# Performance work log

Hardware: AMD Instinct MI355X
Metric: run time of the kernel (lower is better)

Reference implementation:

```python
import jax, jax.numpy as jnp
import numpy as np

N_NODES, N_EDGES, N_GRAPHS = 65536, 131072, 2048
F_NODE, F_EDGE, DIM, DIM1, DIM2 = 78, 10, 256, 512, 256
FP_DIM, FP2, FP3, NCB = 1489, 128, 256, 2

PNAMES = []
for _l in (1, 2, 3):
    PNAMES += [f"e{_l}w", f"e{_l}b", f"n{_l}w1", f"n{_l}b1", f"n{_l}w2", f"n{_l}b2",
               f"bn{_l}g", f"bn{_l}b", f"bn{_l}m", f"bn{_l}v"]
PNAMES += ["fcg_w", "fcg_b", "fp1_w", "fp1_b", "fp2_w", "fp2_b",
           "fb1_w", "fb1_b", "fb2_w", "fb2_b", "fb3_w", "fb3_b", "fb4_w", "fb4_b"]


def _params(key):
    ks = iter(jax.random.split(key, 64))
    def rn(*s):
        return jax.random.normal(next(ks), s, dtype=jnp.float32) * 0.05
    def ru(*s):
        return jax.random.uniform(next(ks), s, dtype=jnp.float32)
    p = {}
    for l, ci in zip((1, 2, 3), (F_NODE, DIM1, DIM1)):
        h = DIM if l == 1 else DIM1
        p[f"e{l}w"] = rn(ci, F_EDGE); p[f"e{l}b"] = rn(ci)          # GINEConv edge lin: 10 -> in_channels
        p[f"n{l}w1"] = rn(h, ci);     p[f"n{l}b1"] = rn(h)
        p[f"n{l}w2"] = rn(DIM1, h);   p[f"n{l}b2"] = rn(DIM1)
        p[f"bn{l}g"] = ru(DIM1) + 0.5; p[f"bn{l}b"] = rn(DIM1)
        p[f"bn{l}m"] = rn(DIM1);       p[f"bn{l}v"] = ru(DIM1) + 0.5
    p["fcg_w"] = rn(DIM2, DIM1);  p["fcg_b"] = rn(DIM2)
    p["fp1_w"] = rn(FP2, FP_DIM); p["fp1_b"] = rn(FP2)
    p["fp2_w"] = rn(FP3, FP2);    p["fp2_b"] = rn(FP3)
    for i, (o, ci) in enumerate([(256, 512), (128, 256), (64, 128), (NCB, 64)], 1):
        p[f"fb{i}_w"] = rn(o, ci); p[f"fb{i}_b"] = rn(o)
    return p


def setup_inputs() -> dict:
    key = jax.random.key(0)
    k = jax.random.split(key, 6)
    inp = {
        "x": jax.random.normal(k[0], (N_NODES, F_NODE), dtype=jnp.float32),
        "finger": jax.random.uniform(k[1], (N_GRAPHS, FP_DIM), dtype=jnp.float32),
        "edge_attr": jax.random.normal(k[2], (N_EDGES, F_EDGE), dtype=jnp.float32),
        "edge_index": jax.random.randint(k[3], (2, N_EDGES), 0, N_NODES),
        "batch": jnp.sort(jax.random.randint(k[4], (N_NODES,), 0, N_GRAPHS)),
    }
    inp.update(_params(k[5]))
    return inp


def _lin(x, w, b):
    return x @ w.T + b


def _bn(x, g, b, m, v):
    # eval-mode BatchNorm1d with running stats
    return (x - m) * jax.lax.rsqrt(v + 1e-5) * g + b


def _forward(x, finger, edge_attr, edge_index, batch, p):
    src, dst = edge_index[0], edge_index[1]
    h = x
    for l in (1, 2, 3):
        # GINEConv (eps=0): out = nn(x + sum_j relu(x_j + lin(edge_attr)))
        e = _lin(edge_attr, p[f"e{l}w"], p[f"e{l}b"])               # [E, Cin]
        m = jax.nn.relu(h[src] + e)                                   # gather + edge add
        agg = jax.ops.segment_sum(m, dst, num_segments=N_NODES)      # scatter-add
        t = h + agg
        t = _lin(jax.nn.relu(_lin(t, p[f"n{l}w1"], p[f"n{l}b1"])), p[f"n{l}w2"], p[f"n{l}b2"])
        h = _bn(jax.nn.relu(t), p[f"bn{l}g"], p[f"bn{l}b"], p[f"bn{l}m"], p[f"bn{l}v"])
    g = jax.ops.segment_sum(h, batch, num_segments=N_GRAPHS)         # global_add_pool
    g = jax.nn.relu(_lin(g, p["fcg_w"], p["fcg_b"]))                 # fc_1 (dropout is eval no-op)
    fp = jax.nn.relu(_lin(finger, p["fp1_w"], p["fp1_b"]))
    fp = jax.nn.relu(_lin(fp, p["fp2_w"], p["fp2_b"]))
    y = jnp.concatenate([g, fp], axis=1)                              # [B, 512]
    for i in (1, 2, 3):
        y = jax.nn.relu(_lin(y, p[f"fb{i}_w"], p[f"fb{i}_b"]))
    y = _lin(y, p["fb4_w"], p["fb4_b"])
    return jax.nn.sigmoid(y)


def reference(x, finger, edge_attr, edge_index, batch,
              e1w, e1b, n1w1, n1b1, n1w2, n1b2, bn1g, bn1b, bn1m, bn1v,
              e2w, e2b, n2w1, n2b1, n2w2, n2b2, bn2g, bn2b, bn2m, bn2v,
              e3w, e3b, n3w1, n3b1, n3w2, n3b2, bn3g, bn3b, bn3m, bn3v,
              fcg_w, fcg_b, fp1_w, fp1_b, fp2_w, fp2_b,
              fb1_w, fb1_b, fb2_w, fb2_b, fb3_w, fb3_b, fb4_w, fb4_b):
    args = dict(locals())
    p = {k: args[k] for k in PNAMES}
    return _forward(x, finger, edge_attr, edge_index, batch, p)
```

## Files before the change

kernel.cpp:

```cpp
#include <hip/hip_runtime.h>
#include <stdint.h>

typedef unsigned short u16;
typedef unsigned int u32;
typedef __bf16 bf16x8 __attribute__((ext_vector_type(8)));
typedef float f32x4 __attribute__((ext_vector_type(4)));
typedef _Float16 h2 __attribute__((ext_vector_type(2)));

#define N_NODES 65536
#define N_EDGES 131072
#define N_GRAPHS 2048

static __device__ __forceinline__ float bf2f(u16 u) {
  union { u32 u; float f; } v; v.u = ((u32)u) << 16; return v.f;
}
static __device__ __forceinline__ u16 f2bf(float f) {
  union { float f; u32 u; } v; v.f = f;
  u32 r = v.u + 0x7fffu + ((v.u >> 16) & 1u);
  return (u16)(r >> 16);
}
static __device__ __forceinline__ void gl16(const void* g, void* l) {
  __builtin_amdgcn_global_load_lds(
      (__attribute__((address_space(1))) void*)(g),
      (__attribute__((address_space(3))) void*)(l), 16, 0, 0);
}
static __device__ __forceinline__ h2 b2h2(u32 u) {
  union { u32 u; h2 h; } v; v.u = u; return v.h;
}
static __device__ __forceinline__ u32 pk2h(float a, float b) {
  union { _Float16 h[2]; u32 u; } v;
  v.h[0] = (_Float16)a; v.h[1] = (_Float16)b; return v.u;
}
#if __has_builtin(__builtin_amdgcn_fdot2)
#define FDOT2(a, b, c) __builtin_amdgcn_fdot2((a), (b), (c), false)
#else
#define FDOT2(a, b, c) \
  ((c) + (float)(a)[0] * (float)(b)[0] + (float)(a)[1] * (float)(b)[1])
#endif

template <int EPI>
__global__ __launch_bounds__(256) void gemm_bt128(
    const u16* __restrict__ A, const u16* __restrict__ W,
    const float* __restrict__ bias, const float* __restrict__ scale,
    const float* __restrict__ shift, u16* __restrict__ Cp,
    int K, int ldc) {
  __shared__ u16 As[128 * 128];
  __shared__ u16 Bs[128 * 128];
  const u32 gx = gridDim.x;
  const u32 nwg = gx * gridDim.y;
  u32 lid = blockIdx.y * gx + blockIdx.x;
  if ((nwg & 7u) == 0u) {
    const u32 cpx = nwg >> 3;
    lid = (lid & 7u) * cpx + (lid >> 3);
  }
  const int bm = (int)(lid / gx) * 128;
  const int bn = (int)(lid % gx) * 128;
  const int tid = threadIdx.x;
  const int lane = tid & 63;
  const int wid = tid >> 6;
  const int wr = wid >> 1, wc = wid & 1;
  const int lg = lane >> 4, lr = lane & 15;

  f32x4 acc[4][4];
#pragma unroll
  for (int i = 0; i < 4; ++i)
#pragma unroll
    for (int j = 0; j < 4; ++j) acc[i][j] = (f32x4){0.f, 0.f, 0.f, 0.f};

  const int srow16 = tid >> 4;
  const int gslot = ((tid & 15) ^ srow16) * 8;
  const u16* Ag[8];
  const u16* Wg[8];
#pragma unroll
  for (int p = 0; p < 8; ++p) {
    Ag[p] = A + (size_t)(bm + p * 16 + srow16) * K + gslot;
    Wg[p] = W + (size_t)(bn + p * 16 + srow16) * K + gslot;
  }
  u16* dA = &As[tid * 8];
  u16* dB = &Bs[tid * 8];

  for (int k0 = 0; k0 < K; k0 += 128) {
#pragma unroll
    for (int p = 0; p < 8; ++p) {
      gl16(Ag[p] + k0, dA + p * 2048);
      gl16(Wg[p] + k0, dB + p * 2048);
    }
    __syncthreads();
#pragma unroll
    for (int kk = 0; kk < 4; ++kk) {
      const int slot = ((kk * 4 + lg) ^ lr) * 8;
      bf16x8 af[4], bfv[4];
#pragma unroll
      for (int i = 0; i < 4; ++i)
        af[i] = *(const bf16x8*)&As[(wr * 64 + i * 16 + lr) * 128 + slot];
#pragma unroll
      for (int j = 0; j < 4; ++j)
        bfv[j] = *(const bf16x8*)&Bs[(wc * 64 + j * 16 + lr) * 128 + slot];
#pragma unroll
      for (int i = 0; i < 4; ++i)
#pragma unroll
        for (int j = 0; j < 4; ++j)
          acc[i][j] = __builtin_amdgcn_mfma_f32_16x16x32_bf16(
              af[i], bfv[j], acc[i][j], 0, 0, 0);
    }
    __syncthreads();
  }

#pragma unroll
  for (int i = 0; i < 4; ++i) {
#pragma unroll
    for (int j = 0; j < 4; ++j) {
#pragma unroll
      for (int r = 0; r < 4; ++r) {
        const int grow = bm + wr * 64 + i * 16 + lg * 4 + r;
        const int gcol = bn + wc * 64 + j * 16 + lr;
        float v = acc[i][j][r] + bias[gcol];
        v = fmaxf(v, 0.f);
        if (EPI == 1) v = v * scale[gcol] + shift[gcol];
        Cp[(size_t)grow * ldc + gcol] = f2bf(v);
      }
    }
  }
}

template <int EPI>
__global__ __launch_bounds__(256) void gemm_bt(
    const u16* __restrict__ A, const u16* __restrict__ W,
    const float* __restrict__ bias, const float* __restrict__ scale,
    const float* __restrict__ shift, u16* __restrict__ Cp,
    int K, int ldc, int coff) {
  __shared__ u16 As[128 * 32];
  __shared__ u16 Bs[128 * 32];
  const u32 gx = gridDim.x;
  const u32 nwg = gx * gridDim.y;
  u32 lid = blockIdx.y * gx + blockIdx.x;
  if ((nwg & 7u) == 0u) {
    const u32 cpx = nwg >> 3;
    lid = (lid & 7u) * cpx + (lid >> 3);
  }
  const int bm = (int)(lid / gx) * 128;
  const int bn = (int)(lid % gx) * 128;
  const int tid = threadIdx.x;
  const int lane = tid & 63;
  const int wid = tid >> 6;
  const int wr = wid >> 1, wc = wid & 1;
  const int lg = lane >> 4, lr = lane & 15;

  f32x4 acc[4][4];
#pragma unroll
  for (int i = 0; i < 4; ++i)
#pragma unroll
    for (int j = 0; j < 4; ++j) acc[i][j] = (f32x4){0.f, 0.f, 0.f, 0.f};

  const int srow = tid >> 2;
  const int c8 = (tid & 3) * 8;
  const u16* Ag0 = A + (size_t)(bm + srow) * K + c8;
  const u16* Ag1 = A + (size_t)(bm + 64 + srow) * K + c8;
  const u16* Wg0 = W + (size_t)(bn + srow) * K + c8;
  const u16* Wg1 = W + (size_t)(bn + 64 + srow) * K + c8;
  u16* lA0 = &As[tid * 8];
  u16* lA1 = &As[2048 + tid * 8];
  u16* lB0 = &Bs[tid * 8];
  u16* lB1 = &Bs[2048 + tid * 8];

  for (int k0 = 0; k0 < K; k0 += 32) {
    gl16(Ag0 + k0, lA0);
    gl16(Ag1 + k0, lA1);
    gl16(Wg0 + k0, lB0);
    gl16(Wg1 + k0, lB1);
    __syncthreads();
    bf16x8 af[4], bfv[4];
#pragma unroll
    for (int i = 0; i < 4; ++i)
      af[i] = *(const bf16x8*)&As[(wr * 64 + i * 16 + lr) * 32 + lg * 8];
#pragma unroll
    for (int j = 0; j < 4; ++j)
      bfv[j] = *(const bf16x8*)&Bs[(wc * 64 + j * 16 + lr) * 32 + lg * 8];
#pragma unroll
    for (int i = 0; i < 4; ++i)
#pragma unroll
      for (int j = 0; j < 4; ++j)
        acc[i][j] = __builtin_amdgcn_mfma_f32_16x16x32_bf16(af[i], bfv[j],
                                                            acc[i][j], 0, 0, 0);
    __syncthreads();
  }

#pragma unroll
  for (int i = 0; i < 4; ++i) {
#pragma unroll
    for (int j = 0; j < 4; ++j) {
#pragma unroll
      for (int r = 0; r < 4; ++r) {
        const int grow = bm + wr * 64 + i * 16 + lg * 4 + r;
        const int gcol = bn + wc * 64 + j * 16 + lr;
        float v = acc[i][j][r] + bias[gcol];
        v = fmaxf(v, 0.f);
        if (EPI == 1) v = v * scale[gcol] + shift[gcol];
        Cp[(size_t)grow * ldc + coff + gcol] = f2bf(v);
      }
    }
  }
}

__global__ void hist_deg(const int* __restrict__ dst, int* __restrict__ deg) {
  int e = blockIdx.x * blockDim.x + threadIdx.x;
  if (e < N_EDGES) atomicAdd(&deg[dst[e]], 1);
}

__global__ __launch_bounds__(1024) void scan_rowptr(const int* __restrict__ deg,
                                                    int* __restrict__ rowptr) {
  __shared__ int lds[1024];
  const int t = threadIdx.x;
  const int base = t * 64;
  int s = 0;
  for (int i = 0; i < 64; ++i) s += deg[base + i];
  lds[t] = s;
  __syncthreads();
  for (int ofs = 1; ofs < 1024; ofs <<= 1) {
    int v = (t >= ofs) ? lds[t - ofs] : 0;
    __syncthreads();
    lds[t] += v;
    __syncthreads();
  }
  int run = (t == 0) ? 0 : lds[t - 1];
  for (int i = 0; i < 64; ++i) {
    rowptr[base + i] = run;
    run += deg[base + i];
  }
  if (t == 1023) rowptr[65536] = run;
}

__global__ void scatter_csr(const int* __restrict__ dst,
                            const int* __restrict__ rowptr,
                            int* __restrict__ deg, int* __restrict__ csr) {
  int e = blockIdx.x * blockDim.x + threadIdx.x;
  if (e >= N_EDGES) return;
  int d = dst[e];
  int pos = atomicSub(&deg[d], 1) - 1;
  csr[rowptr[d] + pos] = e;
}

__global__ void prep_edges(const int* __restrict__ csr,
                           const int* __restrict__ esrc,
                           const float* __restrict__ ea,
                           int* __restrict__ src_s, u32* __restrict__ ea16) {
  int i = blockIdx.x * blockDim.x + threadIdx.x;
  if (i >= N_EDGES) return;
  const int eid = csr[i];
  src_s[i] = esrc[eid];
  const float* er = ea + (size_t)eid * 10;
  u32* o = ea16 + (size_t)i * 5;
  o[0] = pk2h(er[0], er[1]);
  o[1] = pk2h(er[2], er[3]);
  o[2] = pk2h(er[4], er[5]);
  o[3] = pk2h(er[6], er[7]);
  o[4] = pk2h(er[8], er[9]);
}

__global__ void ew_h16(const float* __restrict__ ew1, const float* __restrict__ ew2,
                       const float* __restrict__ ew3, u32* __restrict__ o1,
                       u32* __restrict__ o2, u32* __restrict__ o3) {
  int i = blockIdx.x * blockDim.x + threadIdx.x;
  const float* src;
  u32* dst;
  if (i < 512) { src = ew2 + (size_t)i * 10; dst = o2 + i * 5; }
  else if (i < 1024) { src = ew3 + (size_t)(i - 512) * 10; dst = o3 + (i - 512) * 5; }
  else if (i < 1102) { src = ew1 + (size_t)(i - 1024) * 10; dst = o1 + (i - 1024) * 5; }
  else return;
#pragma unroll
  for (int k = 0; k < 5; ++k) dst[k] = pk2h(src[2 * k], src[2 * k + 1]);
}

__global__ __launch_bounds__(128) void gather512d(
    const int* __restrict__ rowptr, const int* __restrict__ src_s,
    const u32* __restrict__ ea16, const u32* __restrict__ ew16,
    const float* __restrict__ eb, const u16* __restrict__ H,
    u16* __restrict__ T) {
  const int t = threadIdx.x;
  const int c4 = t * 4;
  h2 w[4][5];
#pragma unroll
  for (int j = 0; j < 4; ++j)
#pragma unroll
    for (int k = 0; k < 5; ++k) w[j][k] = b2h2(ew16[(c4 + j) * 5 + k]);
  float eb4[4];
#pragma unroll
  for (int j = 0; j < 4; ++j) eb4[j] = eb[c4 + j];

  const int dend = blockIdx.x * 8 + 8;
  for (int d = blockIdx.x * 8; d < dend; ++d) {
    uint2 hv = *(const uint2*)&H[(size_t)d * 512 + c4];
    float a0 = bf2f((u16)(hv.x & 0xffffu)), a1 = bf2f((u16)(hv.x >> 16));
    float a2 = bf2f((u16)(hv.y & 0xffffu)), a3 = bf2f((u16)(hv.y >> 16));
    const int i1 = rowptr[d + 1];
#pragma unroll 2
    for (int i = rowptr[d]; i < i1; ++i) {
      const int s = src_s[i];
      const u32* ep = ea16 + (size_t)i * 5;
      const h2 e0 = b2h2(ep[0]), e1 = b2h2(ep[1]), e2 = b2h2(ep[2]),
               e3 = b2h2(ep[3]), e4 = b2h2(ep[4]);
      uint2 hs = *(const uint2*)&H[(size_t)s * 512 + c4];
      float h0 = bf2f((u16)(hs.x & 0xffffu)), h1 = bf2f((u16)(hs.x >> 16));
      float h2v = bf2f((u16)(hs.y & 0xffffu)), h3 = bf2f((u16)(hs.y >> 16));
      float l0 = eb4[0], l1 = eb4[1], l2 = eb4[2], l3 = eb4[3];
      l0 = FDOT2(e0, w[0][0], l0); l0 = FDOT2(e1, w[0][1], l0);
      l0 = FDOT2(e2, w[0][2], l0); l0 = FDOT2(e3, w[0][3], l0);
      l0 = FDOT2(e4, w[0][4], l0);
      l1 = FDOT2(e0, w[1][0], l1); l1 = FDOT2(e1, w[1][1], l1);
      l1 = FDOT2(e2, w[1][2], l1); l1 = FDOT2(e3, w[1][3], l1);
      l1 = FDOT2(e4, w[1][4], l1);
      l2 = FDOT2(e0, w[2][0], l2); l2 = FDOT2(e1, w[2][1], l2);
      l2 = FDOT2(e2, w[2][2], l2); l2 = FDOT2(e3, w[2][3], l2);
      l2 = FDOT2(e4, w[2][4], l2);
      l3 = FDOT2(e0, w[3][0], l3); l3 = FDOT2(e1, w[3][1], l3);
      l3 = FDOT2(e2, w[3][2], l3); l3 = FDOT2(e3, w[3][3], l3);
      l3 = FDOT2(e4, w[3][4], l3);
      a0 += fmaxf(h0 + l0, 0.f);
      a1 += fmaxf(h1 + l1, 0.f);
      a2 += fmaxf(h2v + l2, 0.f);
      a3 += fmaxf(h3 + l3, 0.f);
    }
    uint2 r;
    r.x = (u32)f2bf(a0) | ((u32)f2bf(a1) << 16);
    r.y = (u32)f2bf(a2) | ((u32)f2bf(a3) << 16);
    *(uint2*)&T[(size_t)d * 512 + c4] = r;
  }
}

__global__ __launch_bounds__(128) void gather78d(
    const int* __restrict__ rowptr, const int* __restrict__ src_s,
    const u32* __restrict__ ea16, const u32* __restrict__ ew16,
    const float* __restrict__ eb, const float* __restrict__ X,
    u16* __restrict__ T) {
  const int t = threadIdx.x;
  const bool act = t < 78;
  h2 w[5];
  float ebv = 0.f;
  if (act) {
#pragma unroll
    for (int k = 0; k < 5; ++k) w[k] = b2h2(ew16[t * 5 + k]);
    ebv = eb[t];
  }
  const int dend = blockIdx.x * 8 + 8;
  for (int d = blockIdx.x * 8; d < dend; ++d) {
    float acc = act ? X[(size_t)d * 78 + t] : 0.f;
    const int i1 = rowptr[d + 1];
    for (int i = rowptr[d]; i < i1; ++i) {
      const int s = src_s[i];
      const u32* ep = ea16 + (size_t)i * 5;
      const h2 e0 = b2h2(ep[0]), e1 = b2h2(ep[1]), e2 = b2h2(ep[2]),
               e3 = b2h2(ep[3]), e4 = b2h2(ep[4]);
      if (act) {
        float el = ebv;
        el = FDOT2(e0, w[0], el); el = FDOT2(e1, w[1], el);
        el = FDOT2(e2, w[2], el); el = FDOT2(e3, w[3], el);
        el = FDOT2(e4, w[4], el);
        acc += fmaxf(X[(size_t)s * 78 + t] + el, 0.f);
      }
    }
    if (t < 96) T[(size_t)d * 96 + t] = act ? f2bf(acc) : (u16)0;
  }
}

struct CvtJob { const float* in; u16* out; int cin; int cout; };
struct CvtJobs { CvtJob j[11]; int blk_ofs[12]; };

__global__ __launch_bounds__(256) void cvt_multi(CvtJobs jb, int njobs) {
  int b = blockIdx.x;
  int ji = 0;
  while (ji + 1 < njobs && b >= jb.blk_ofs[ji + 1]) ++ji;
  const CvtJob J = jb.j[ji];
  int idx = (b - jb.blk_ofs[ji]) * 256 + threadIdx.x;
  int r = idx / J.cout, c = idx - r * J.cout;
  int tot_blocks = jb.blk_ofs[ji + 1] - jb.blk_ofs[ji];
  if (idx >= tot_blocks * 256) return;
  if (idx >= ((tot_blocks * 256) / J.cout) * J.cout && c >= J.cout) return;
  J.out[idx] = (c < J.cin) ? f2bf(J.in[(size_t)r * J.cin + c]) : (u16)0;
}

struct BnJobs { const float* g[3]; const float* b[3]; const float* m[3];
                const float* v[3]; };
__global__ void bn_affine3(BnJobs p, float* __restrict__ bnS) {
  int i = blockIdx.x * blockDim.x + threadIdx.x;
  int l = i >> 9, c = i & 511;
  float s = p.g[l][c] * rsqrtf(p.v[l][c] + 1e-5f);
  bnS[l * 1024 + c] = s;
  bnS[l * 1024 + 512 + c] = p.b[l][c] - p.m[l][c] * s;
}

__global__ void seg_starts(const int* __restrict__ batch, int* __restrict__ start,
                           int n, int ngraphs) {
  int i = blockIdx.x * blockDim.x + threadIdx.x;
  if (i >= n) return;
  int b = batch[i];
  int prev = (i == 0) ? -1 : batch[i - 1];
  for (int g = prev + 1; g <= b; ++g) start[g] = i;
  if (i == n - 1)
    for (int g = b + 1; g <= ngraphs; ++g) start[g] = n;
}

__global__ void cvt_pad(const float* __restrict__ in, u16* __restrict__ out,
                        int rows, int cin, int cout) {
  int idx = blockIdx.x * blockDim.x + threadIdx.x;
  if (idx >= rows * cout) return;
  int rrow = idx / cout, j = idx - rrow * cout;
  out[idx] = (j < cin) ? f2bf(in[(size_t)rrow * cin + j]) : (u16)0;
}

__global__ void pool_sum(const u16* __restrict__ H, const int* __restrict__ start,
                         u16* __restrict__ g) {
  int gi = blockIdx.x, c = threadIdx.x;
  int s = start[gi], e = start[gi + 1];
  float acc = 0.f;
  for (int i = s; i < e; ++i) acc += bf2f(H[(size_t)i * 512 + c]);
  g[gi * 512 + c] = f2bf(acc);
}

__global__ void fb34(const u16* __restrict__ y2, const float* __restrict__ w3,
                     const float* __restrict__ b3, const float* __restrict__ w4,
                     const float* __restrict__ b4, float* __restrict__ out) {
  __shared__ float yr[128];
  __shared__ float h3[64];
  const int row = blockIdx.x, t = threadIdx.x;
  yr[t] = bf2f(y2[row * 128 + t]);
  yr[t + 64] = bf2f(y2[row * 128 + 64 + t]);
  __syncthreads();
  float s = b3[t];
  const float* w3r = &w3[t * 128];
#pragma unroll 8
  for (int k = 0; k < 128; ++k) s += yr[k] * w3r[k];
  h3[t] = fmaxf(s, 0.f);
  __syncthreads();
  if (t < 2) {
    float s4 = b4[t];
    const float* w4r = &w4[t * 64];
    for (int k = 0; k < 64; ++k) s4 += h3[k] * w4r[k];
    out[row * 2 + t] = 1.f / (1.f + expf(-s4));
  }
}

#define CDIV(a, b) (((a) + (b)-1) / (b))

extern "C" void kernel_launch(void* const* d_in, const int* in_sizes, int n_in,
                              void* d_out, int out_size, void* d_ws, size_t ws_size,
                              hipStream_t stream) {
  const float* x = (const float*)d_in[0];
  const float* finger = (const float*)d_in[1];
  const float* ea = (const float*)d_in[2];
  const int* eidx = (const int*)d_in[3];
  const int* batch = (const int*)d_in[4];
  const int* esrc = eidx;
  const int* edst = eidx + N_EDGES;

  const float* P[49];
  for (int i = 5; i < 49; ++i) P[i] = (const float*)d_in[i];
  const float* fcg_w = P[35]; const float* fcg_b = P[36];
  const float* fp1_w = P[37]; const float* fp1_b = P[38];
  const float* fp2_w = P[39]; const float* fp2_b = P[40];
  const float* fb1_w = P[41]; const float* fb1_b = P[42];
  const float* fb2_w = P[43]; const float* fb2_b = P[44];
  const float* fb3_w = P[45]; const float* fb3_b = P[46];
  const float* fb4_w = P[47]; const float* fb4_b = P[48];

  size_t off = 0;
  char* base = (char*)d_ws;
  auto alloc = [&](size_t bytes) -> void* {
    void* p = base + off;
    off = (off + bytes + 255) & ~(size_t)255;
    return p;
  };
  char* BA = (char*)alloc((size_t)N_NODES * 512 * 2);
  char* BB = (char*)alloc((size_t)N_NODES * 512 * 2);
  u16* w11 = (u16*)alloc(256 * 96 * 2);
  u16* w12 = (u16*)alloc(512 * 256 * 2);
  u16* w21 = (u16*)alloc(512 * 512 * 2);
  u16* w22 = (u16*)alloc(512 * 512 * 2);
  u16* w31 = (u16*)alloc(512 * 512 * 2);
  u16* w32 = (u16*)alloc(512 * 512 * 2);
  u16* wfcg = (u16*)alloc(256 * 512 * 2);
  u16* wfp1 = (u16*)alloc(128 * 1504 * 2);
  u16* wfp2 = (u16*)alloc(256 * 128 * 2);
  u16* wfb1 = (u16*)alloc(256 * 512 * 2);
  u16* wfb2 = (u16*)alloc(128 * 256 * 2);
  float* bnS = (float*)alloc(6 * 512 * 4);
  int* start = (int*)alloc(2049 * 4);
  int* deg = (int*)alloc(65536 * 4);
  int* rowptr = (int*)alloc(65537 * 4);
  int* csr = (int*)alloc(131072 * 4);
  int* src_s = (int*)alloc(131072 * 4);
  u32* ea16 = (u32*)alloc((size_t)131072 * 5 * 4);
  u32* ew16a = (u32*)alloc(512 * 5 * 4);
  u32* ew16b = (u32*)alloc(512 * 5 * 4);
  u32* ew16c = (u32*)alloc(128 * 5 * 4);
  if (off > ws_size) return;

  u16* fingb = (u16*)BA;
  u16* gbuf = (u16*)(BA + 6160384);
  u16* y0 = (u16*)(BA + 8257536);
  u16* fpa = (u16*)(BA + 10354688);
  u16* y1 = (u16*)(BA + 10878976);
  u16* y2 = (u16*)(BA + 11927552);

  {
    CvtJobs jb;
    const float* ins[11] = {P[5 + 2], P[5 + 4], P[15 + 2], P[15 + 4], P[25 + 2],
                            P[25 + 4], fcg_w, fp1_w, fp2_w, fb1_w, fb2_w};
    u16* outs[11] = {w11, w12, w21, w22, w31, w32, wfcg, wfp1, wfp2, wfb1, wfb2};
    int rows[11] = {256, 512, 512, 512, 512, 512, 256, 128, 256, 256, 128};
    int cins[11] = {78, 256, 512, 512, 512, 512, 512, 1489, 128, 512, 256};
    int couts[11] = {96, 256, 512, 512, 512, 512, 512, 1504, 128, 512, 256};
    int acc = 0;
    for (int i = 0; i < 11; ++i) {
      jb.j[i].in = ins[i]; jb.j[i].out = outs[i];
      jb.j[i].cin = cins[i]; jb.j[i].cout = couts[i];
      jb.blk_ofs[i] = acc;
      acc += CDIV(rows[i] * couts[i], 256);
    }
    jb.blk_ofs[11] = acc;
    cvt_multi<<<acc, 256, 0, stream>>>(jb, 11);
  }
  {
    BnJobs bj;
    for (int l = 0; l < 3; ++l) {
      int pb = 5 + 10 * l;
      bj.g[l] = P[pb + 6]; bj.b[l] = P[pb + 7];
      bj.m[l] = P[pb + 8]; bj.v[l] = P[pb + 9];
    }
    bn_affine3<<<6, 256, 0, stream>>>(bj, bnS);
  }
  seg_starts<<<CDIV(N_NODES, 256), 256, 0, stream>>>(batch, start, N_NODES, N_GRAPHS);
  ew_h16<<<5, 256, 0, stream>>>(P[5], P[15], P[25], ew16c, ew16a, ew16b);

  hipMemsetAsync(deg, 0, 65536 * 4, stream);
  hist_deg<<<CDIV(N_EDGES, 256), 256, 0, stream>>>(edst, deg);
  scan_rowptr<<<1, 1024, 0, stream>>>(deg, rowptr);
  scatter_csr<<<CDIV(N_EDGES, 256), 256, 0, stream>>>(edst, rowptr, deg, csr);
  prep_edges<<<CDIV(N_EDGES, 256), 256, 0, stream>>>(csr, esrc, ea, src_s, ea16);

  gather78d<<<N_NODES / 8, 128, 0, stream>>>(rowptr, src_s, ea16, ew16c, P[6], x,
                                             (u16*)BB);
  gemm_bt<0><<<dim3(2, 512), 256, 0, stream>>>((u16*)BB, w11, P[5 + 3], nullptr,
                                               nullptr, (u16*)BA, 96, 256, 0);
  gemm_bt128<1><<<dim3(4, 512), 256, 0, stream>>>((u16*)BA, w12, P[5 + 5], bnS,
                                                  bnS + 512, (u16*)BB, 256, 512);

  gather512d<<<N_NODES / 8, 128, 0, stream>>>(rowptr, src_s, ea16, ew16a, P[16],
                                              (const u16*)BB, (u16*)BA);
  gemm_bt128<0><<<dim3(4, 512), 256, 0, stream>>>((u16*)BA, w21, P[15 + 3], nullptr,
                                                  nullptr, (u16*)BB, 512, 512);
  gemm_bt128<1><<<dim3(4, 512), 256, 0, stream>>>((u16*)BB, w22, P[15 + 5],
                                                  bnS + 1024, bnS + 1024 + 512,
                                                  (u16*)BA, 512, 512);

  gather512d<<<N_NODES / 8, 128, 0, stream>>>(rowptr, src_s, ea16, ew16b, P[26],
                                              (const u16*)BA, (u16*)BB);
  gemm_bt128<0><<<dim3(4, 512), 256, 0, stream>>>((u16*)BB, w31, P[25 + 3], nullptr,
                                                  nullptr, (u16*)BA, 512, 512);
  gemm_bt128<1><<<dim3(4, 512), 256, 0, stream>>>((u16*)BA, w32, P[25 + 5],
                                                  bnS + 2048, bnS + 2048 + 512,
                                                  (u16*)BB, 512, 512);

  pool_sum<<<N_GRAPHS, 512, 0, stream>>>((const u16*)BB, start, gbuf);
  cvt_pad<<<CDIV(N_GRAPHS * 1504, 256), 256, 0, stream>>>(finger, fingb, N_GRAPHS,
                                                          1489, 1504);
  gemm_bt<0><<<dim3(2, 16), 256, 0, stream>>>(gbuf, wfcg, fcg_b, nullptr, nullptr,
                                              y0, 512, 512, 0);
  gemm_bt<0><<<dim3(1, 16), 256, 0, stream>>>(fingb, wfp1, fp1_b, nullptr, nullptr,
                                              fpa, 1504, 128, 0);
  gemm_bt<0><<<dim3(2, 16), 256, 0, stream>>>(fpa, wfp2, fp2_b, nullptr, nullptr,
                                              y0, 128, 512, 256);
  gemm_bt<0><<<dim3(2, 16), 256, 0, stream>>>(y0, wfb1, fb1_b, nullptr, nullptr,
                                              y1, 512, 256, 0);
  gemm_bt<0><<<dim3(1, 16), 256, 0, stream>>>(y1, wfb2, fb2_b, nullptr, nullptr,
                                              y2, 256, 128, 0);
  fb34<<<N_GRAPHS, 64, 0, stream>>>(y2, fb3_w, fb3_b, fb4_w, fb4_b, (float*)d_out);
}
```

Baseline: 536.5 us.

## Fuse graph-level MLP head into one kernel with LDS-resident intermediates

Replaces the six separate head launches (fc_g, two fingerprint linears, fb1, fb2, fb34) with a single kernel. Each 512-thread block handles 16 graphs and keeps intermediate activations in shared memory between MFMA stages. fb3 also moves to bf16 MFMA, which needs an extra weight conversion job. This removes launch overhead and global round-trips for the small head GEMMs. In exchange there are only 128 blocks, each re-reading weights directly from global memory, and fb3 runs at lower precision.

```diff
diff --git a/kernel.cpp b/kernel.cpp
--- a/kernel.cpp
+++ b/kernel.cpp
@@ -199,6 +199,132 @@
         Cp[(size_t)grow * ldc + coff + gcol] = f2bf(v);
       }
     }
+  }
+}
+
+static __device__ __forceinline__ void head_stage2(
+    const u16* Sa, u16* So, int kofs, const u16* __restrict__ W, int ldw,
+    const float* __restrict__ bias, int KT, int w, int l, int lr, int lg) {
+  f32x4 acc[2];
+  acc[0] = (f32x4){0.f, 0.f, 0.f, 0.f};
+  acc[1] = (f32x4){0.f, 0.f, 0.f, 0.f};
+  for (int t = 0; t < KT; ++t) {
+    bf16x8 a = *(const bf16x8*)&Sa[t * 512 + l * 8];
+#pragma unroll
+    for (int j = 0; j < 2; ++j) {
+      bf16x8 b = *(const bf16x8*)&W[(size_t)(w * 32 + j * 16 + lr) * ldw +
+                                    t * 32 + lg * 8];
+      acc[j] = __builtin_amdgcn_mfma_f32_16x16x32_bf16(b, a, acc[j], 0, 0, 0);
+    }
+  }
+#pragma unroll
+  for (int j = 0; j < 2; ++j) {
+    const int c0 = w * 32 + j * 16 + lg * 4;
+    const float4 bs = *(const float4*)&bias[c0];
+    const float v0 = fmaxf(acc[j][0] + bs.x, 0.f);
+    const float v1 = fmaxf(acc[j][1] + bs.y, 0.f);
+    const float v2 = fmaxf(acc[j][2] + bs.z, 0.f);
+    const float v3 = fmaxf(acc[j][3] + bs.w, 0.f);
+    uint2 r;
+    r.x = (u32)f2bf(v0) | ((u32)f2bf(v1) << 16);
+    r.y = (u32)f2bf(v2) | ((u32)f2bf(v3) << 16);
+    const int k0 = kofs + c0;
+    *(uint2*)&So[(k0 >> 5) * 512 + ((k0 & 31) >> 3) * 128 + lr * 8 + (k0 & 7)] = r;
+  }
+}
+
+static __device__ __forceinline__ void head_stage1(
+    const u16* Sa, u16* So, int kofs, const u16* __restrict__ W, int ldw,
+    const float* __restrict__ bias, int KT, int w, int l, int lr, int lg) {
+  f32x4 acc = (f32x4){0.f, 0.f, 0.f, 0.f};
+  for (int t = 0; t < KT; ++t) {
+    bf16x8 a = *(const bf16x8*)&Sa[t * 512 + l * 8];
+    bf16x8 b = *(const bf16x8*)&W[(size_t)(w * 16 + lr) * ldw + t * 32 + lg * 8];
+    acc = __builtin_amdgcn_mfma_f32_16x16x32_bf16(b, a, acc, 0, 0, 0);
+  }
+  const int c0 = w * 16 + lg * 4;
+  const float4 bs = *(const float4*)&bias[c0];
+  const float v0 = fmaxf(acc[0] + bs.x, 0.f);
+  const float v1 = fmaxf(acc[1] + bs.y, 0.f);
+  const float v2 = fmaxf(acc[2] + bs.z, 0.f);
+  const float v3 = fmaxf(acc[3] + bs.w, 0.f);
+  uint2 r;
+  r.x = (u32)f2bf(v0) | ((u32)f2bf(v1) << 16);
+  r.y = (u32)f2bf(v2) | ((u32)f2bf(v3) << 16);
+  const int k0 = kofs + c0;
+  *(uint2*)&So[(k0 >> 5) * 512 + ((k0 & 31) >> 3) * 128 + lr * 8 + (k0 & 7)] = r;
+}
+
+__global__ __launch_bounds__(512) void head_fused(
+    const u16* __restrict__ gbuf, const u16* __restrict__ fingb,
+    const u16* __restrict__ wfcg, const float* __restrict__ fcg_b,
+    const u16* __restrict__ wfp1, const float* __restrict__ fp1_b,
+    const u16* __restrict__ wfp2, const float* __restrict__ fp2_b,
+    const u16* __restrict__ wfb1, const float* __restrict__ fb1_b,
+    const u16* __restrict__ wfb2, const float* __restrict__ fb2_b,
+    const u16* __restrict__ wfb3, const float* __restrict__ fb3_b,
+    const float* __restrict__ fb4_w, const float* __restrict__ fb4_b,
+    float* __restrict__ out) {
+  __shared__ u16 S[26624];
+  const int g0 = blockIdx.x * 16;
+  const int tid = threadIdx.x;
+  const int w = tid >> 6, l = tid & 63;
+  const int lr = l & 15, lg = l >> 4;
+
+  for (int v = tid; v < 1024; v += 512) {
+    const int r = v >> 6, c0 = (v & 63) * 8;
+    uint4 d = *(const uint4*)&gbuf[(size_t)(g0 + r) * 512 + c0];
+    *(uint4*)&S[(c0 >> 5) * 512 + ((c0 & 31) >> 3) * 128 + r * 8] = d;
+  }
+  __syncthreads();
+  head_stage2(&S[0], &S[8192], 0, wfcg, 512, fcg_b, 16, w, l, lr, lg);
+  {
+    f32x4 acc = (f32x4){0.f, 0.f, 0.f, 0.f};
+    for (int t = 0; t < 47; ++t) {
+      bf16x8 a = *(const bf16x8*)&fingb[(size_t)(g0 + lr) * 1504 + t * 32 + lg * 8];
+      bf16x8 b = *(const bf16x8*)&wfp1[(size_t)(w * 16 + lr) * 1504 + t * 32 + lg * 8];
+      acc = __builtin_amdgcn_mfma_f32_16x16x32_bf16(b, a, acc, 0, 0, 0);
+    }
+    const int c0 = w * 16 + lg * 4;
+    const float4 bs = *(const float4*)&fp1_b[c0];
+    const float v0 = fmaxf(acc[0] + bs.x, 0.f);
+    const float v1 = fmaxf(acc[1] + bs.y, 0.f);
+    const float v2 = fmaxf(acc[2] + bs.z, 0.f);
+    const float v3 = fmaxf(acc[3] + bs.w, 0.f);
+    uint2 r;
+    r.x = (u32)f2bf(v0) | ((u32)f2bf(v1) << 16);
+    r.y = (u32)f2bf(v2) | ((u32)f2bf(v3) << 16);
+    *(uint2*)&S[16384 + (c0 >> 5) * 512 + ((c0 & 31) >> 3) * 128 + lr * 8 +
+                (c0 & 7)] = r;
+  }
+  __syncthreads();
+  head_stage2(&S[16384], &S[8192], 256, wfp2, 128, fp2_b, 4, w, l, lr, lg);
+  __syncthreads();
+  head_stage2(&S[8192], &S[18432], 0, wfb1, 512, fb1_b, 16, w, l, lr, lg);
+  __syncthreads();
+  head_stage1(&S[18432], &S[22528], 0, wfb2, 256, fb2_b, 8, w, l, lr, lg);
+  __syncthreads();
+  if (w < 4) {
+    f32x4 acc = (f32x4){0.f, 0.f, 0.f, 0.f};
+    for (int t = 0; t < 4; ++t) {
+      bf16x8 a = *(const bf16x8*)&S[22528 + t * 512 + l * 8];
+      bf16x8 b = *(const bf16x8*)&wfb3[(size_t)(w * 16 + lr) * 128 + t * 32 + lg * 8];
+      acc = __builtin_amdgcn_mfma_f32_16x16x32_bf16(b, a, acc, 0, 0, 0);
+    }
+    const int c0 = w * 16 + lg * 4;
+    float* H3 = (float*)&S[24576];
+#pragma unroll
+    for (int r = 0; r < 4; ++r)
+      H3[lr * 64 + c0 + r] = fmaxf(acc[r] + fb3_b[c0 + r], 0.f);
+  }
+  __syncthreads();
+  if (tid < 32) {
+    const int r = tid >> 1, o = tid & 1;
+    const float* H3 = (const float*)&S[24576];
+    float s = fb4_b[o];
+#pragma unroll 8
+    for (int k = 0; k < 64; ++k) s += H3[r * 64 + k] * fb4_w[o * 64 + k];
+    out[(size_t)(g0 + r) * 2 + o] = 1.f / (1.f + expf(-s));
   }
 }
 
@@ -363,7 +489,7 @@
 }
 
 struct CvtJob { const float* in; u16* out; int cin; int cout; };
-struct CvtJobs { CvtJob j[11]; int blk_ofs[12]; };
+struct CvtJobs { CvtJob j[12]; int blk_ofs[13]; };
 
 __global__ __launch_bounds__(256) void cvt_multi(CvtJobs jb, int njobs) {
   int b = blockIdx.x;
@@ -414,29 +540,6 @@
   float acc = 0.f;
   for (int i = s; i < e; ++i) acc += bf2f(H[(size_t)i * 512 + c]);
   g[gi * 512 + c] = f2bf(acc);
-}
-
-__global__ void fb34(const u16* __restrict__ y2, const float* __restrict__ w3,
-                     const float* __restrict__ b3, const float* __restrict__ w4,
-                     const float* __restrict__ b4, float* __restrict__ out) {
-  __shared__ float yr[128];
-  __shared__ float h3[64];
-  const int row = blockIdx.x, t = threadIdx.x;
-  yr[t] = bf2f(y2[row * 128 + t]);
-  yr[t + 64] = bf2f(y2[row * 128 + 64 + t]);
-  __syncthreads();
-  float s = b3[t];
-  const float* w3r = &w3[t * 128];
-#pragma unroll 8
-  for (int k = 0; k < 128; ++k) s += yr[k] * w3r[k];
-  h3[t] = fmaxf(s, 0.f);
-  __syncthreads();
-  if (t < 2) {
-    float s4 = b4[t];
-    const float* w4r = &w4[t * 64];
-    for (int k = 0; k < 64; ++k) s4 += h3[k] * w4r[k];
-    out[row * 2 + t] = 1.f / (1.f + expf(-s4));
-  }
 }
 
 #define CDIV(a, b) (((a) + (b)-1) / (b))
@@ -482,6 +585,7 @@
   u16* wfp2 = (u16*)alloc(256 * 128 * 2);
   u16* wfb1 = (u16*)alloc(256 * 512 * 2);
   u16* wfb2 = (u16*)alloc(128 * 256 * 2);
+  u16* wfb3 = (u16*)alloc(64 * 128 * 2);
   float* bnS = (float*)alloc(6 * 512 * 4);
   int* start = (int*)alloc(2049 * 4);
   int* deg = (int*)alloc(65536 * 4);
@@ -496,28 +600,25 @@
 
   u16* fingb = (u16*)BA;
   u16* gbuf = (u16*)(BA + 6160384);
-  u16* y0 = (u16*)(BA + 8257536);
-  u16* fpa = (u16*)(BA + 10354688);
-  u16* y1 = (u16*)(BA + 10878976);
-  u16* y2 = (u16*)(BA + 11927552);
 
   {
     CvtJobs jb;
-    const float* ins[11] = {P[5 + 2], P[5 + 4], P[15 + 2], P[15 + 4], P[25 + 2],
-                            P[25 + 4], fcg_w, fp1_w, fp2_w, fb1_w, fb2_w};
-    u16* outs[11] = {w11, w12, w21, w22, w31, w32, wfcg, wfp1, wfp2, wfb1, wfb2};
-    int rows[11] = {256, 512, 512, 512, 512, 512, 256, 128, 256, 256, 128};
-    int cins[11] = {78, 256, 512, 512, 512, 512, 512, 1489, 128, 512, 256};
-    int couts[11] = {96, 256, 512, 512, 512, 512, 512, 1504, 128, 512, 256};
+    const float* ins[12] = {P[5 + 2], P[5 + 4], P[15 + 2], P[15 + 4], P[25 + 2],
+                            P[25 + 4], fcg_w, fp1_w, fp2_w, fb1_w, fb2_w, fb3_w};
+    u16* outs[12] = {w11, w12, w21, w22, w31, w32, wfcg, wfp1, wfp2, wfb1,
+                     wfb2, wfb3};
+    int rows[12] = {256, 512, 512, 512, 512, 512, 256, 128, 256, 256, 128, 64};
+    int cins[12] = {78, 256, 512, 512, 512, 512, 512, 1489, 128, 512, 256, 128};
+    int couts[12] = {96, 256, 512, 512, 512, 512, 512, 1504, 128, 512, 256, 128};
     int acc = 0;
-    for (int i = 0; i < 11; ++i) {
+    for (int i = 0; i < 12; ++i) {
       jb.j[i].in = ins[i]; jb.j[i].out = outs[i];
       jb.j[i].cin = cins[i]; jb.j[i].cout = couts[i];
       jb.blk_ofs[i] = acc;
       acc += CDIV(rows[i] * couts[i], 256);
     }
-    jb.blk_ofs[11] = acc;
-    cvt_multi<<<acc, 256, 0, stream>>>(jb, 11);
+    jb.blk_ofs[12] = acc;
+    cvt_multi<<<acc, 256, 0, stream>>>(jb, 12);
   }
   {
     BnJobs bj;
@@ -563,15 +664,7 @@
   pool_sum<<<N_GRAPHS, 512, 0, stream>>>((const u16*)BB, start, gbuf);
   cvt_pad<<<CDIV(N_GRAPHS * 1504, 256), 256, 0, stream>>>(finger, fingb, N_GRAPHS,
                                                           1489, 1504);
-  gemm_bt<0><<<dim3(2, 16), 256, 0, stream>>>(gbuf, wfcg, fcg_b, nullptr, nullptr,
-                                              y0, 512, 512, 0);
-  gemm_bt<0><<<dim3(1, 16), 256, 0, stream>>>(fingb, wfp1, fp1_b, nullptr, nullptr,
-                                              fpa, 1504, 128, 0);
-  gemm_bt<0><<<dim3(2, 16), 256, 0, stream>>>(fpa, wfp2, fp2_b, nullptr, nullptr,
-                                              y0, 128, 512, 256);
-  gemm_bt<0><<<dim3(2, 16), 256, 0, stream>>>(y0, wfb1, fb1_b, nullptr, nullptr,
-                                              y1, 512, 256, 0);
-  gemm_bt<0><<<dim3(1, 16), 256, 0, stream>>>(y1, wfb2, fb2_b, nullptr, nullptr,
-                                              y2, 256, 128, 0);
-  fb34<<<N_GRAPHS, 64, 0, stream>>>(y2, fb3_w, fb3_b, fb4_w, fb4_b, (float*)d_out);
-}
+  head_fused<<<N_GRAPHS / 16, 512, 0, stream>>>(
+      gbuf, fingb, wfcg, fcg_b, wfp1, fp1_b, wfp2, fp2_b, wfb1, fb1_b, wfb2,
+      fb2_b, wfb3, fb3_b, fb4_w, fb4_b, (float*)d_out);
+}
```

Measured after the change: 482.5 us, median of 3. 1.11x faster.
